# Kernel optimization log

Measured on AMD Instinct MI355X. Metric: run time of the kernel, lower is better.

Reference implementation:

```python
import jax, jax.numpy as jnp
import numpy as np

D_MODEL = 64
N_HEAD = 8
MAX_REL = 16  # module hardcodes max_relative_position = 16
B, S = 8, 1024


def _linear_params(k, fan_in, fan_out):
    kw, kb = jax.random.split(k)
    s = 1.0 / np.sqrt(fan_in)
    W = jax.random.uniform(kw, (fan_in, fan_out), jnp.float32, -s, s)
    b = jax.random.uniform(kb, (fan_out,), jnp.float32, -s, s)
    return W, b


def setup_inputs() -> dict:
    key = jax.random.key(0)
    ks = jax.random.split(key, 10)
    Wq, bq = _linear_params(ks[0], D_MODEL, D_MODEL * N_HEAD)
    Wk, bk = _linear_params(ks[1], D_MODEL, D_MODEL * N_HEAD)
    Wv, bv = _linear_params(ks[2], D_MODEL, D_MODEL * N_HEAD)
    Wo, bo = _linear_params(ks[3], D_MODEL * N_HEAD, D_MODEL)
    Wkr, bkr = _linear_params(ks[4], D_MODEL, D_MODEL)
    Wqr, bqr = _linear_params(ks[5], D_MODEL, D_MODEL)
    p = jax.random.normal(ks[6], (2 * MAX_REL + 1, D_MODEL), jnp.float32)
    query = jax.random.normal(ks[7], (B, S, D_MODEL), jnp.float32)
    key_t = jax.random.normal(ks[8], (B, S, D_MODEL), jnp.float32)
    value = jax.random.normal(ks[9], (B, S, D_MODEL), jnp.float32)
    return dict(query=query, key=key_t, value=value,
                Wq=Wq, bq=bq, Wk=Wk, bk=bk, Wv=Wv, bv=bv,
                Wo=Wo, bo=bo, Wkr=Wkr, bkr=bkr, Wqr=Wqr, bqr=bqr, p=p)


def reference(query, key, value, Wq, bq, Wk, bk, Wv, bv, Wo, bo, Wkr, bkr, Wqr, bqr, p):
    Bsz, Sq, d = query.shape
    H = Wq.shape[1] // d  # head_dim == d_model in this module
    scale = jnp.sqrt(jnp.asarray(3 * d, jnp.float32))

    def heads(x, W, b):
        return (x @ W + b).reshape(Bsz, -1, H, d).transpose(0, 2, 1, 3)  # [B,H,S,d]

    q1 = heads(query, Wq, bq)
    k1 = heads(key, Wk, bk)
    v1 = heads(value, Wv, bv)

    # content-content term
    attn1 = jnp.einsum('bhqd,bhkd->bhqk', q1, k1)

    # relative-position terms. make_table uses clamp(dist, min=16, max=16)+16,
    # so every gather index is exactly 2*MAX_REL -> the gathered value is the
    # single column 2*MAX_REL of each table, broadcast over the last axis.
    k_r = p @ Wkr + bkr  # [2*MAX_REL+1, d]
    q_r = p @ Wqr + bqr
    attn2 = jnp.einsum('bhqd,d->bhq', q1, k_r[2 * MAX_REL])[..., None]  # [B,H,Sq,1]
    attn3 = jnp.einsum('bhkd,d->bhk', k1, q_r[2 * MAX_REL])[..., None]  # [B,H,Sk,1] (Sk==Sq)

    attn = jax.nn.softmax((attn1 + attn2 + attn3) / scale, axis=-1)
    x = jnp.einsum('bhqk,bhkd->bhqd', attn, v1)
    x = x.transpose(0, 2, 1, 3).reshape(Bsz, Sq, H * d)
    return x @ Wo + bo
```

## Files before the change

### kernel.cpp

```cpp
#include <hip/hip_runtime.h>
#include <hip/hip_bf16.h>


#define N_HEAD 8
#define BATCH  8
#define SEQ    1024
#define DMH    512
#define SC2    0.10411804386480816f

typedef __hip_bfloat16 bf16;
typedef __bf16 bf16x8 __attribute__((ext_vector_type(8)));
typedef __bf16 bf16x4 __attribute__((ext_vector_type(4)));
typedef float  f32x4  __attribute__((ext_vector_type(4)));

__global__ __launch_bounds__(256)
void init_kernel(const float* __restrict__ Wq, const float* __restrict__ Wk,
                 const float* __restrict__ Wv, const float* __restrict__ Wo,
                 const float* __restrict__ bo, float* __restrict__ out,
                 bf16* __restrict__ WqT, bf16* __restrict__ WkT,
                 bf16* __restrict__ WvT, bf16* __restrict__ WoT)
{
    const int idx = blockIdx.x * 256 + threadIdx.x;
    out[idx] = bo[idx & 63];
    if (idx < 512 * 64) {
        {
            const int n = idx >> 6, k = idx & 63;
            WqT[idx] = __float2bfloat16(Wq[(size_t)k * 512 + n]);
            WkT[idx] = __float2bfloat16(Wk[(size_t)k * 512 + n]);
            WvT[idx] = __float2bfloat16(Wv[(size_t)k * 512 + n]);
        }
        {
            const int c = idx >> 9, k = idx & 511;
            WoT[idx] = __float2bfloat16(Wo[(size_t)k * 64 + c]);
        }
    }
}

__global__ __launch_bounds__(256)
void qkv_mfma_kernel(const float* __restrict__ Xq, const float* __restrict__ Xk,
                     const float* __restrict__ Xv,
                     const bf16* __restrict__ WqT, const bf16* __restrict__ WkT,
                     const bf16* __restrict__ WvT,
                     const float* __restrict__ bq, const float* __restrict__ bk,
                     const float* __restrict__ bv,
                     bf16* __restrict__ Qh, bf16* __restrict__ Kh,
                     bf16* __restrict__ Vt)
{
    const int rt    = blockIdx.x;
    const int ct    = blockIdx.y;
    const int which = blockIdx.z;

    const float* __restrict__ X    = which == 0 ? Xq  : (which == 1 ? Xk  : Xv);
    const bf16*  __restrict__ WT   = which == 0 ? WqT : (which == 1 ? WkT : WvT);
    const float* __restrict__ bias = which == 0 ? bq  : (which == 1 ? bk  : bv);

    __shared__ __align__(16) bf16 Xs [128 * 72];
    __shared__ __align__(16) bf16 Wts[64 * 72];
    __shared__ float Bs[64];

    const int tid  = threadIdx.x;
    const int w4   = tid >> 6;
    const int lane = tid & 63;
    const int t16  = lane & 15;
    const int quad = lane >> 4;

    if (tid < 64) Bs[tid] = bias[ct * 64 + tid];
    for (int i = tid; i < 2048; i += 256) {
        const int r = i >> 4, c4 = (i & 15) << 2;
        const float4 v = *(const float4*)&X[(size_t)(rt * 128 + r) * 64 + c4];
        bf16 t[4] = {__float2bfloat16(v.x), __float2bfloat16(v.y),
                     __float2bfloat16(v.z), __float2bfloat16(v.w)};
        *(bf16x4*)&Xs[r * 72 + c4] = *(bf16x4*)t;
    }
    for (int i = tid; i < 512; i += 256) {
        const int r8 = i >> 3, c8 = (i & 7) << 3;
        *(bf16x8*)&Wts[r8 * 72 + c8] = *(const bf16x8*)&WT[(size_t)(ct * 64 + r8) * 64 + c8];
    }
    __syncthreads();

    bf16x8 bf0[4], bf1[4];
#pragma unroll
    for (int nt = 0; nt < 4; nt++) {
        bf0[nt] = *(const bf16x8*)&Wts[(nt * 16 + t16) * 72 + 0  + quad * 8];
        bf1[nt] = *(const bf16x8*)&Wts[(nt * 16 + t16) * 72 + 32 + quad * 8];
    }

    f32x4 acc[2][4];
#pragma unroll
    for (int rs = 0; rs < 2; rs++) {
        const int m = rs * 64 + w4 * 16 + t16;
        const bf16x8 af0 = *(const bf16x8*)&Xs[m * 72 + 0  + quad * 8];
        const bf16x8 af1 = *(const bf16x8*)&Xs[m * 72 + 32 + quad * 8];
#pragma unroll
        for (int nt = 0; nt < 4; nt++) {
            acc[rs][nt] = (f32x4){0.f, 0.f, 0.f, 0.f};
            acc[rs][nt] = __builtin_amdgcn_mfma_f32_16x16x32_bf16(af0, bf0[nt], acc[rs][nt], 0, 0, 0);
            acc[rs][nt] = __builtin_amdgcn_mfma_f32_16x16x32_bf16(af1, bf1[nt], acc[rs][nt], 0, 0, 0);
        }
    }

    const int b     = rt >> 3;
    const int sbase = (rt & 7) * 128;

    if (which < 2) {
        bf16* O = which == 0 ? Qh : Kh;
        const float sc = (which == 0) ? SC2 : 1.0f;
#pragma unroll
        for (int rs = 0; rs < 2; rs++)
#pragma unroll
            for (int rr = 0; rr < 4; rr++) {
                const int s = sbase + rs * 64 + w4 * 16 + quad * 4 + rr;
                bf16* dst = O + (((size_t)b * N_HEAD + ct) * SEQ + s) * 64 + t16;
#pragma unroll
                for (int nt = 0; nt < 4; nt++)
                    dst[nt * 16] = __float2bfloat16((acc[rs][nt][rr] + Bs[nt * 16 + t16]) * sc);
            }
    } else {
        __syncthreads();
        bf16* VtS = Xs;
#pragma unroll
        for (int rs = 0; rs < 2; rs++)
#pragma unroll
            for (int nt = 0; nt < 4; nt++)
#pragma unroll
                for (int rr = 0; rr < 4; rr++) {
                    const int rloc = rs * 64 + w4 * 16 + quad * 4 + rr;
                    VtS[(nt * 16 + t16) * 136 + rloc] =
                        __float2bfloat16(acc[rs][nt][rr] + Bs[nt * 16 + t16]);
                }
        __syncthreads();
        for (int i = tid; i < 1024; i += 256) {
            const int c = i >> 4, r8 = (i & 15) << 3;
            *(bf16x8*)&Vt[(((size_t)b * N_HEAD + ct) * 64 + c) * SEQ + sbase + r8] =
                *(const bf16x8*)&VtS[c * 136 + r8];
        }
    }
}

__global__ __launch_bounds__(512, 4)
void flash_attn_kernel(const bf16* __restrict__ Qh, const bf16* __restrict__ Kh,
                       const bf16* __restrict__ Vt, const bf16* __restrict__ WoT,
                       float* __restrict__ out)
{
    const int qt   = blockIdx.x;
    const int h    = blockIdx.y;
    const int b    = blockIdx.z;
    const int tid  = threadIdx.x;
    const int wave = tid >> 6;
    const int w4   = wave & 3;
    const int kh   = wave >> 2;
    const int lane = tid & 63;
    const int t16  = lane & 15;
    const int quad = lane >> 4;

    const size_t bh = (size_t)b * N_HEAD + h;
    const bf16* __restrict__ Qp  = Qh + bh * (SEQ * 64);
    const bf16* __restrict__ Kp  = Kh + bh * (SEQ * 64);
    const bf16* __restrict__ Vtp = Vt + bh * (64 * SEQ);

    __shared__ __align__(16) bf16 smem[36864];
    bf16* KsB  = smem;
    bf16* VtsB = smem + 9216;
    bf16* PsB  = smem + 18432;

    bf16x8 qf0[2], qf1[2];
#pragma unroll
    for (int rs = 0; rs < 2; rs++) {
        const int qrow = qt * 128 + rs * 64 + w4 * 16 + t16;
        qf0[rs] = *(const bf16x8*)(Qp + (size_t)qrow * 64 + 0  + quad * 8);
        qf1[rs] = *(const bf16x8*)(Qp + (size_t)qrow * 64 + 32 + quad * 8);
    }

    f32x4 Of[2][4];
    float l_i[2][4];
#pragma unroll
    for (int rs = 0; rs < 2; rs++) {
#pragma unroll
        for (int nt = 0; nt < 4; nt++) Of[rs][nt] = (f32x4){0.f, 0.f, 0.f, 0.f};
#pragma unroll
        for (int rr = 0; rr < 4; rr++) l_i[rs][rr] = 0.f;
    }

    for (int kt = 0; kt < 8; kt++) {
#pragma unroll
        for (int i = tid; i < 2048; i += 512) {
            const int khs = i >> 10;
            const int j   = i & 1023;
            const int vk  = j >> 9;
            const int r8  = (j & 511) >> 3;
            const int c8  = (j & 7) << 3;
            if (vk == 0)
                *(bf16x8*)&KsB[khs * 4608 + r8 * 72 + c8] =
                    *(const bf16x8*)&Kp[(size_t)(khs * 512 + kt * 64 + r8) * 64 + c8];
            else
                *(bf16x8*)&VtsB[khs * 4608 + r8 * 72 + c8] =
                    *(const bf16x8*)&Vtp[(size_t)r8 * SEQ + khs * 512 + kt * 64 + c8];
        }
        __syncthreads();

        const bf16* Ksw  = KsB  + kh * 4608;
        const bf16* Vtsw = VtsB + kh * 4608;

#pragma unroll
        for (int rs = 0; rs < 2; rs++) {
            f32x4 Sf[4];
#pragma unroll
            for (int nt = 0; nt < 4; nt++) {
                Sf[nt] = (f32x4){0.f, 0.f, 0.f, 0.f};
                const bf16x8 kf0 = *(const bf16x8*)&Ksw[(nt * 16 + t16) * 72 + 0  + quad * 8];
                const bf16x8 kf1 = *(const bf16x8*)&Ksw[(nt * 16 + t16) * 72 + 32 + quad * 8];
                Sf[nt] = __builtin_amdgcn_mfma_f32_16x16x32_bf16(qf0[rs], kf0, Sf[nt], 0, 0, 0);
                Sf[nt] = __builtin_amdgcn_mfma_f32_16x16x32_bf16(qf1[rs], kf1, Sf[nt], 0, 0, 0);
            }

#pragma unroll
            for (int nt = 0; nt < 4; nt++)
#pragma unroll
                for (int rr = 0; rr < 4; rr++) {
                    const float p = exp2f(Sf[nt][rr]);
                    Sf[nt][rr] = p;
                    l_i[rs][rr] += p;
                }

            bf16* Psw = PsB + (rs * 8 + wave) * 1152;
#pragma unroll
            for (int nt = 0; nt < 4; nt++)
#pragma unroll
                for (int rr = 0; rr < 4; rr++)
                    Psw[(quad * 4 + rr) * 72 + nt * 16 + t16] =
                        __float2bfloat16(Sf[nt][rr]);

            const bf16x8 pf0 = *(const bf16x8*)&Psw[t16 * 72 + 0  + quad * 8];
            const bf16x8 pf1 = *(const bf16x8*)&Psw[t16 * 72 + 32 + quad * 8];
#pragma unroll
            for (int nt = 0; nt < 4; nt++) {
                const bf16x8 vf0 = *(const bf16x8*)&Vtsw[(nt * 16 + t16) * 72 + 0  + quad * 8];
                const bf16x8 vf1 = *(const bf16x8*)&Vtsw[(nt * 16 + t16) * 72 + 32 + quad * 8];
                Of[rs][nt] = __builtin_amdgcn_mfma_f32_16x16x32_bf16(pf0, vf0, Of[rs][nt], 0, 0, 0);
                Of[rs][nt] = __builtin_amdgcn_mfma_f32_16x16x32_bf16(pf1, vf1, Of[rs][nt], 0, 0, 0);
            }
        }
        __syncthreads();
    }

    float* Xch = (float*)smem;
    float* Lch = (float*)(smem + 16384);
    bf16*  WoS = smem + 20480;
    bf16*  Pe  = smem + 25088;

    if (kh == 1) {
#pragma unroll
        for (int rs = 0; rs < 2; rs++) {
#pragma unroll
            for (int nt = 0; nt < 4; nt++)
#pragma unroll
                for (int rr = 0; rr < 4; rr++)
                    Xch[((w4 * 2 + rs) * 64 + lane) * 16 + nt * 4 + rr] = Of[rs][nt][rr];
#pragma unroll
            for (int rr = 0; rr < 4; rr++)
                Lch[((w4 * 2 + rs) * 64 + lane) * 4 + rr] = l_i[rs][rr];
        }
    }
    {
        const int r8 = tid >> 3, c8 = (tid & 7) << 3;
        *(bf16x8*)&WoS[r8 * 72 + c8] = *(const bf16x8*)&WoT[(size_t)r8 * 512 + h * 64 + c8];
    }
    __syncthreads();

    if (kh == 0) {
#pragma unroll
        for (int rs = 0; rs < 2; rs++) {
#pragma unroll
            for (int nt = 0; nt < 4; nt++)
#pragma unroll
                for (int rr = 0; rr < 4; rr++)
                    Of[rs][nt][rr] += Xch[((w4 * 2 + rs) * 64 + lane) * 16 + nt * 4 + rr];
#pragma unroll
            for (int rr = 0; rr < 4; rr++)
                l_i[rs][rr] += Lch[((w4 * 2 + rs) * 64 + lane) * 4 + rr];
        }

#pragma unroll
        for (int rs = 0; rs < 2; rs++)
#pragma unroll
            for (int off = 8; off >= 1; off >>= 1)
#pragma unroll
                for (int rr = 0; rr < 4; rr++)
                    l_i[rs][rr] += __shfl_xor(l_i[rs][rr], off, 64);

        bf16* Pew = Pe + w4 * 1152;
#pragma unroll
        for (int rs = 0; rs < 2; rs++) {
            float inv_l[4];
#pragma unroll
            for (int rr = 0; rr < 4; rr++) inv_l[rr] = 1.0f / l_i[rs][rr];
#pragma unroll
            for (int nt = 0; nt < 4; nt++)
#pragma unroll
                for (int rr = 0; rr < 4; rr++)
                    Pew[(quad * 4 + rr) * 72 + nt * 16 + t16] =
                        __float2bfloat16(Of[rs][nt][rr] * inv_l[rr]);

            const bf16x8 pf0 = *(const bf16x8*)&Pew[t16 * 72 + 0  + quad * 8];
            const bf16x8 pf1 = *(const bf16x8*)&Pew[t16 * 72 + 32 + quad * 8];

            f32x4 R[4];
#pragma unroll
            for (int nt = 0; nt < 4; nt++) {
                R[nt] = (f32x4){0.f, 0.f, 0.f, 0.f};
                const bf16x8 wf0 = *(const bf16x8*)&WoS[(nt * 16 + t16) * 72 + 0  + quad * 8];
                const bf16x8 wf1 = *(const bf16x8*)&WoS[(nt * 16 + t16) * 72 + 32 + quad * 8];
                R[nt] = __builtin_amdgcn_mfma_f32_16x16x32_bf16(pf0, wf0, R[nt], 0, 0, 0);
                R[nt] = __builtin_amdgcn_mfma_f32_16x16x32_bf16(pf1, wf1, R[nt], 0, 0, 0);
            }

            const int srow_base = qt * 128 + rs * 64 + w4 * 16 + quad * 4;
#pragma unroll
            for (int rr = 0; rr < 4; rr++) {
                const size_t base = ((size_t)b * SEQ + srow_base + rr) * 64;
#pragma unroll
                for (int nt = 0; nt < 4; nt++)
                    atomicAdd(&out[base + nt * 16 + t16], R[nt][rr]);
            }
        }
    }
}

extern "C" void kernel_launch(void* const* d_in, const int* in_sizes, int n_in,
                              void* d_out, int out_size, void* d_ws, size_t ws_size,
                              hipStream_t stream)
{
    const float* query = (const float*)d_in[0];
    const float* key_  = (const float*)d_in[1];
    const float* value = (const float*)d_in[2];
    const float* Wq    = (const float*)d_in[3];
    const float* bq    = (const float*)d_in[4];
    const float* Wk    = (const float*)d_in[5];
    const float* bk    = (const float*)d_in[6];
    const float* Wv    = (const float*)d_in[7];
    const float* bv    = (const float*)d_in[8];
    const float* Wo    = (const float*)d_in[9];
    const float* bo    = (const float*)d_in[10];

    float* out = (float*)d_out;
    char* ws   = (char*)d_ws;
    bf16* Qh  = (bf16*)(ws + (size_t) 0 * 1024 * 1024);
    bf16* Kh  = (bf16*)(ws + (size_t) 8 * 1024 * 1024);
    bf16* Vt  = (bf16*)(ws + (size_t)16 * 1024 * 1024);
    bf16* WoT = (bf16*)(ws + (size_t)24 * 1024 * 1024);
    bf16* WqT = (bf16*)(ws + (size_t)24 * 1024 * 1024 + 65536);
    bf16* WkT = (bf16*)(ws + (size_t)24 * 1024 * 1024 + 131072);
    bf16* WvT = (bf16*)(ws + (size_t)24 * 1024 * 1024 + 196608);

    init_kernel<<<dim3(2048), 256, 0, stream>>>(Wq, Wk, Wv, Wo, bo, out,
                                                WqT, WkT, WvT, WoT);
    qkv_mfma_kernel<<<dim3(64, 8, 3), 256, 0, stream>>>(
        query, key_, value, WqT, WkT, WvT, bq, bk, bv, Qh, Kh, Vt);
    flash_attn_kernel<<<dim3(8, 8, 8), 512, 0, stream>>>(Qh, Kh, Vt, WoT, out);
}
```

Before: 147.7 us.

## Restructure QKV projection per row tile, prefetch K/V tiles in attention, reorder grid

The QKV projection kernel now gives each block a 64-row tile of X and loops over all 8 heads, reading weights straight from global memory. The input is converted to bf16 once per row tile instead of once per head, and the bias smem staging goes away. The flash attention kernel now register-prefetches the next K/V tile while the current tile is being computed, hiding global load latency behind the MFMA work. The attention grid is also reordered so the batch-head index is fastest, which changes L2 locality. The cost is fewer, longer-running projection blocks, more registers for the prefetch buffers, and weight fragments coming from global memory rather than LDS.

Measured after the change: 154.9 us. 4.9% more time.

```diff
diff --git a/kernel.cpp b/kernel.cpp
--- a/kernel.cpp
+++ b/kernel.cpp
@@ -47,16 +47,14 @@
                      bf16* __restrict__ Vt)
 {
     const int rt    = blockIdx.x;
-    const int ct    = blockIdx.y;
-    const int which = blockIdx.z;
+    const int which = blockIdx.y;
 
     const float* __restrict__ X    = which == 0 ? Xq  : (which == 1 ? Xk  : Xv);
     const bf16*  __restrict__ WT   = which == 0 ? WqT : (which == 1 ? WkT : WvT);
     const float* __restrict__ bias = which == 0 ? bq  : (which == 1 ? bk  : bv);
 
-    __shared__ __align__(16) bf16 Xs [128 * 72];
-    __shared__ __align__(16) bf16 Wts[64 * 72];
-    __shared__ float Bs[64];
+    __shared__ __align__(16) bf16 Xs [64 * 72];
+    __shared__ __align__(16) bf16 VtS[64 * 72];
 
     const int tid  = threadIdx.x;
     const int w4   = tid >> 6;
@@ -64,75 +62,66 @@
     const int t16  = lane & 15;
     const int quad = lane >> 4;
 
-    if (tid < 64) Bs[tid] = bias[ct * 64 + tid];
-    for (int i = tid; i < 2048; i += 256) {
+    for (int i = tid; i < 1024; i += 256) {
         const int r = i >> 4, c4 = (i & 15) << 2;
-        const float4 v = *(const float4*)&X[(size_t)(rt * 128 + r) * 64 + c4];
+        const float4 v = *(const float4*)&X[(size_t)(rt * 64 + r) * 64 + c4];
         bf16 t[4] = {__float2bfloat16(v.x), __float2bfloat16(v.y),
                      __float2bfloat16(v.z), __float2bfloat16(v.w)};
         *(bf16x4*)&Xs[r * 72 + c4] = *(bf16x4*)t;
     }
-    for (int i = tid; i < 512; i += 256) {
-        const int r8 = i >> 3, c8 = (i & 7) << 3;
-        *(bf16x8*)&Wts[r8 * 72 + c8] = *(const bf16x8*)&WT[(size_t)(ct * 64 + r8) * 64 + c8];
-    }
     __syncthreads();
 
-    bf16x8 bf0[4], bf1[4];
-#pragma unroll
-    for (int nt = 0; nt < 4; nt++) {
-        bf0[nt] = *(const bf16x8*)&Wts[(nt * 16 + t16) * 72 + 0  + quad * 8];
-        bf1[nt] = *(const bf16x8*)&Wts[(nt * 16 + t16) * 72 + 32 + quad * 8];
-    }
-
-    f32x4 acc[2][4];
-#pragma unroll
-    for (int rs = 0; rs < 2; rs++) {
-        const int m = rs * 64 + w4 * 16 + t16;
-        const bf16x8 af0 = *(const bf16x8*)&Xs[m * 72 + 0  + quad * 8];
-        const bf16x8 af1 = *(const bf16x8*)&Xs[m * 72 + 32 + quad * 8];
+    const int m = w4 * 16 + t16;
+    const bf16x8 af0 = *(const bf16x8*)&Xs[m * 72 + 0  + quad * 8];
+    const bf16x8 af1 = *(const bf16x8*)&Xs[m * 72 + 32 + quad * 8];
+
+    const int b     = rt >> 4;
+    const int sbase = (rt & 15) * 64;
+
+    for (int ct = 0; ct < N_HEAD; ct++) {
+        bf16x8 bf0[4], bf1[4];
 #pragma unroll
         for (int nt = 0; nt < 4; nt++) {
-            acc[rs][nt] = (f32x4){0.f, 0.f, 0.f, 0.f};
-            acc[rs][nt] = __builtin_amdgcn_mfma_f32_16x16x32_bf16(af0, bf0[nt], acc[rs][nt], 0, 0, 0);
-            acc[rs][nt] = __builtin_amdgcn_mfma_f32_16x16x32_bf16(af1, bf1[nt], acc[rs][nt], 0, 0, 0);
-        }
-    }
-
-    const int b     = rt >> 3;
-    const int sbase = (rt & 7) * 128;
-
-    if (which < 2) {
-        bf16* O = which == 0 ? Qh : Kh;
-        const float sc = (which == 0) ? SC2 : 1.0f;
-#pragma unroll
-        for (int rs = 0; rs < 2; rs++)
+            const size_t base = (size_t)(ct * 64 + nt * 16 + t16) * 64;
+            bf0[nt] = *(const bf16x8*)&WT[base + 0  + quad * 8];
+            bf1[nt] = *(const bf16x8*)&WT[base + 32 + quad * 8];
+        }
+
+        f32x4 acc[4];
+        float bv4[4];
+#pragma unroll
+        for (int nt = 0; nt < 4; nt++) {
+            acc[nt] = (f32x4){0.f, 0.f, 0.f, 0.f};
+            acc[nt] = __builtin_amdgcn_mfma_f32_16x16x32_bf16(af0, bf0[nt], acc[nt], 0, 0, 0);
+            acc[nt] = __builtin_amdgcn_mfma_f32_16x16x32_bf16(af1, bf1[nt], acc[nt], 0, 0, 0);
+            bv4[nt] = bias[ct * 64 + nt * 16 + t16];
+        }
+
+        if (which < 2) {
+            bf16* O = which == 0 ? Qh : Kh;
+            const float sc = (which == 0) ? SC2 : 1.0f;
 #pragma unroll
             for (int rr = 0; rr < 4; rr++) {
-                const int s = sbase + rs * 64 + w4 * 16 + quad * 4 + rr;
+                const int s = sbase + w4 * 16 + quad * 4 + rr;
                 bf16* dst = O + (((size_t)b * N_HEAD + ct) * SEQ + s) * 64 + t16;
 #pragma unroll
                 for (int nt = 0; nt < 4; nt++)
-                    dst[nt * 16] = __float2bfloat16((acc[rs][nt][rr] + Bs[nt * 16 + t16]) * sc);
-            }
-    } else {
-        __syncthreads();
-        bf16* VtS = Xs;
-#pragma unroll
-        for (int rs = 0; rs < 2; rs++)
-#pragma unroll
-            for (int nt = 0; nt < 4; nt++)
-#pragma unroll
-                for (int rr = 0; rr < 4; rr++) {
-                    const int rloc = rs * 64 + w4 * 16 + quad * 4 + rr;
-                    VtS[(nt * 16 + t16) * 136 + rloc] =
-                        __float2bfloat16(acc[rs][nt][rr] + Bs[nt * 16 + t16]);
-                }
-        __syncthreads();
-        for (int i = tid; i < 1024; i += 256) {
-            const int c = i >> 4, r8 = (i & 15) << 3;
-            *(bf16x8*)&Vt[(((size_t)b * N_HEAD + ct) * 64 + c) * SEQ + sbase + r8] =
-                *(const bf16x8*)&VtS[c * 136 + r8];
+                    dst[nt * 16] = __float2bfloat16((acc[nt][rr] + bv4[nt]) * sc);
+            }
+        } else {
+            __syncthreads();
+#pragma unroll
+            for (int nt = 0; nt < 4; nt++)
+#pragma unroll
+                for (int rr = 0; rr < 4; rr++)
+                    VtS[(nt * 16 + t16) * 72 + w4 * 16 + quad * 4 + rr] =
+                        __float2bfloat16(acc[nt][rr] + bv4[nt]);
+            __syncthreads();
+            for (int i = tid; i < 512; i += 256) {
+                const int c = i >> 3, r8 = (i & 7) << 3;
+                *(bf16x8*)&Vt[(((size_t)b * N_HEAD + ct) * 64 + c) * SEQ + sbase + r8] =
+                    *(const bf16x8*)&VtS[c * 72 + r8];
+            }
         }
     }
 }
@@ -142,9 +131,10 @@
                        const bf16* __restrict__ Vt, const bf16* __restrict__ WoT,
                        float* __restrict__ out)
 {
-    const int qt   = blockIdx.x;
-    const int h    = blockIdx.y;
-    const int b    = blockIdx.z;
+    const int bhx  = blockIdx.x;
+    const int qt   = blockIdx.y;
+    const int b    = bhx >> 3;
+    const int h    = bhx & 7;
     const int tid  = threadIdx.x;
     const int wave = tid >> 6;
     const int w4   = wave & 3;
@@ -181,22 +171,27 @@
         for (int rr = 0; rr < 4; rr++) l_i[rs][rr] = 0.f;
     }
 
+    const int r8s = tid >> 3;
+    const int c8s = (tid & 7) << 3;
+    bf16x8 pre[4];
+#define LOAD_TILES(kt_)                                                          \
+    do {                                                                         \
+        pre[0] = *(const bf16x8*)&Kp [(size_t)((kt_) * 64 + r8s) * 64 + c8s];    \
+        pre[1] = *(const bf16x8*)&Vtp[(size_t)r8s * SEQ + (kt_) * 64 + c8s];     \
+        pre[2] = *(const bf16x8*)&Kp [(size_t)(512 + (kt_) * 64 + r8s) * 64 + c8s]; \
+        pre[3] = *(const bf16x8*)&Vtp[(size_t)r8s * SEQ + 512 + (kt_) * 64 + c8s];  \
+    } while (0)
+
+    LOAD_TILES(0);
+
     for (int kt = 0; kt < 8; kt++) {
-#pragma unroll
-        for (int i = tid; i < 2048; i += 512) {
-            const int khs = i >> 10;
-            const int j   = i & 1023;
-            const int vk  = j >> 9;
-            const int r8  = (j & 511) >> 3;
-            const int c8  = (j & 7) << 3;
-            if (vk == 0)
-                *(bf16x8*)&KsB[khs * 4608 + r8 * 72 + c8] =
-                    *(const bf16x8*)&Kp[(size_t)(khs * 512 + kt * 64 + r8) * 64 + c8];
-            else
-                *(bf16x8*)&VtsB[khs * 4608 + r8 * 72 + c8] =
-                    *(const bf16x8*)&Vtp[(size_t)r8 * SEQ + khs * 512 + kt * 64 + c8];
-        }
+        *(bf16x8*)&KsB [       r8s * 72 + c8s] = pre[0];
+        *(bf16x8*)&VtsB[       r8s * 72 + c8s] = pre[1];
+        *(bf16x8*)&KsB [4608 + r8s * 72 + c8s] = pre[2];
+        *(bf16x8*)&VtsB[4608 + r8s * 72 + c8s] = pre[3];
         __syncthreads();
+
+        if (kt < 7) LOAD_TILES(kt + 1);
 
         const bf16* Ksw  = KsB  + kh * 4608;
         const bf16* Vtsw = VtsB + kh * 4608;
@@ -242,6 +237,7 @@
         }
         __syncthreads();
     }
+#undef LOAD_TILES
 
     float* Xch = (float*)smem;
     float* Lch = (float*)(smem + 16384);
@@ -354,7 +350,7 @@
 
     init_kernel<<<dim3(2048), 256, 0, stream>>>(Wq, Wk, Wv, Wo, bo, out,
                                                 WqT, WkT, WvT, WoT);
-    qkv_mfma_kernel<<<dim3(64, 8, 3), 256, 0, stream>>>(
+    qkv_mfma_kernel<<<dim3(128, 3), 256, 0, stream>>>(
         query, key_, value, WqT, WkT, WvT, bq, bk, bv, Qh, Kh, Vt);
-    flash_attn_kernel<<<dim3(8, 8, 8), 512, 0, stream>>>(Qh, Kh, Vt, WoT, out);
+    flash_attn_kernel<<<dim3(64, 8), 512, 0, stream>>>(Qh, Kh, Vt, WoT, out);
 }
```

## Prefetch next K/V tiles into registers and reorder grid for L2 reuse

Applied to the files above, without the earlier changes.

The K/V tile load loop becomes a register-prefetch pipeline: the next tile's global loads are issued right after the barrier so they overlap the current tile's MFMA work. The grid is reordered so consecutive blocks cover different (batch, head) pairs for the same query tile. The cross-half reduction scratch arrays are padded (stride 17/5) to reduce LDS bank conflicts, and the shared-memory offsets are shifted to fit. The prefetch costs extra VGPRs at launch_bounds(512,4), which could cause spills or lower occupancy.

Measured after the change: 145.1 us. About the same (-1.7%).

```diff
diff --git a/kernel.cpp b/kernel.cpp
--- a/kernel.cpp
+++ b/kernel.cpp
@@ -131,7 +131,7 @@
         __syncthreads();
         for (int i = tid; i < 1024; i += 256) {
             const int c = i >> 4, r8 = (i & 15) << 3;
-            *(bf16x8*)&Vt[(((size_t)b * N_HEAD + ct) * 64 + c) * SEQ + sbase + r8] =
+            *(bf16x8*)&Vt[(((size_t)b * N_HEAD + c) * 0 + ((size_t)b * N_HEAD + ct) * 64 + c) * SEQ + sbase + r8] =
                 *(const bf16x8*)&VtS[c * 136 + r8];
         }
     }
@@ -142,9 +142,10 @@
                        const bf16* __restrict__ Vt, const bf16* __restrict__ WoT,
                        float* __restrict__ out)
 {
-    const int qt   = blockIdx.x;
-    const int h    = blockIdx.y;
-    const int b    = blockIdx.z;
+    const int bhx  = blockIdx.x;
+    const int qt   = blockIdx.y;
+    const int b    = bhx >> 3;
+    const int h    = bhx & 7;
     const int tid  = threadIdx.x;
     const int wave = tid >> 6;
     const int w4   = wave & 3;
@@ -181,22 +182,27 @@
         for (int rr = 0; rr < 4; rr++) l_i[rs][rr] = 0.f;
     }
 
+    const int r8s = tid >> 3;
+    const int c8s = (tid & 7) << 3;
+    bf16x8 pre[4];
+#define LOAD_TILES(kt_)                                                          \
+    do {                                                                         \
+        pre[0] = *(const bf16x8*)&Kp [(size_t)((kt_) * 64 + r8s) * 64 + c8s];    \
+        pre[1] = *(const bf16x8*)&Vtp[(size_t)r8s * SEQ + (kt_) * 64 + c8s];     \
+        pre[2] = *(const bf16x8*)&Kp [(size_t)(512 + (kt_) * 64 + r8s) * 64 + c8s]; \
+        pre[3] = *(const bf16x8*)&Vtp[(size_t)r8s * SEQ + 512 + (kt_) * 64 + c8s];  \
+    } while (0)
+
+    LOAD_TILES(0);
+
     for (int kt = 0; kt < 8; kt++) {
-#pragma unroll
-        for (int i = tid; i < 2048; i += 512) {
-            const int khs = i >> 10;
-            const int j   = i & 1023;
-            const int vk  = j >> 9;
-            const int r8  = (j & 511) >> 3;
-            const int c8  = (j & 7) << 3;
-            if (vk == 0)
-                *(bf16x8*)&KsB[khs * 4608 + r8 * 72 + c8] =
-                    *(const bf16x8*)&Kp[(size_t)(khs * 512 + kt * 64 + r8) * 64 + c8];
-            else
-                *(bf16x8*)&VtsB[khs * 4608 + r8 * 72 + c8] =
-                    *(const bf16x8*)&Vtp[(size_t)r8 * SEQ + khs * 512 + kt * 64 + c8];
-        }
+        *(bf16x8*)&KsB [       r8s * 72 + c8s] = pre[0];
+        *(bf16x8*)&VtsB[       r8s * 72 + c8s] = pre[1];
+        *(bf16x8*)&KsB [4608 + r8s * 72 + c8s] = pre[2];
+        *(bf16x8*)&VtsB[4608 + r8s * 72 + c8s] = pre[3];
         __syncthreads();
+
+        if (kt < 7) LOAD_TILES(kt + 1);
 
         const bf16* Ksw  = KsB  + kh * 4608;
         const bf16* Vtsw = VtsB + kh * 4608;
@@ -242,11 +248,12 @@
         }
         __syncthreads();
     }
+#undef LOAD_TILES
 
     float* Xch = (float*)smem;
-    float* Lch = (float*)(smem + 16384);
-    bf16*  WoS = smem + 20480;
-    bf16*  Pe  = smem + 25088;
+    float* Lch = (float*)(smem + 17408);
+    bf16*  WoS = smem + 22528;
+    bf16*  Pe  = smem + 27136;
 
     if (kh == 1) {
 #pragma unroll
@@ -255,10 +262,10 @@
             for (int nt = 0; nt < 4; nt++)
 #pragma unroll
                 for (int rr = 0; rr < 4; rr++)
-                    Xch[((w4 * 2 + rs) * 64 + lane) * 16 + nt * 4 + rr] = Of[rs][nt][rr];
+                    Xch[((w4 * 2 + rs) * 64 + lane) * 17 + nt * 4 + rr] = Of[rs][nt][rr];
 #pragma unroll
             for (int rr = 0; rr < 4; rr++)
-                Lch[((w4 * 2 + rs) * 64 + lane) * 4 + rr] = l_i[rs][rr];
+                Lch[((w4 * 2 + rs) * 64 + lane) * 5 + rr] = l_i[rs][rr];
         }
     }
     {
@@ -274,10 +281,10 @@
             for (int nt = 0; nt < 4; nt++)
 #pragma unroll
                 for (int rr = 0; rr < 4; rr++)
-                    Of[rs][nt][rr] += Xch[((w4 * 2 + rs) * 64 + lane) * 16 + nt * 4 + rr];
+                    Of[rs][nt][rr] += Xch[((w4 * 2 + rs) * 64 + lane) * 17 + nt * 4 + rr];
 #pragma unroll
             for (int rr = 0; rr < 4; rr++)
-                l_i[rs][rr] += Lch[((w4 * 2 + rs) * 64 + lane) * 4 + rr];
+                l_i[rs][rr] += Lch[((w4 * 2 + rs) * 64 + lane) * 5 + rr];
         }
 
 #pragma unroll
@@ -356,5 +363,5 @@
                                                 WqT, WkT, WvT, WoT);
     qkv_mfma_kernel<<<dim3(64, 8, 3), 256, 0, stream>>>(
         query, key_, value, WqT, WkT, WvT, bq, bk, bv, Qh, Kh, Vt);
-    flash_attn_kernel<<<dim3(8, 8, 8), 512, 0, stream>>>(Qh, Kh, Vt, WoT, out);
+    flash_attn_kernel<<<dim3(64, 8), 512, 0, stream>>>(Qh, Kh, Vt, WoT, out);
 }
```
